# Kernel optimization log

Hardware: AMD Instinct MI355X
Metric: run time of the kernel (lower is better)

## Reference

```python
import math
import jax, jax.numpy as jnp
import numpy as np

B, S, D = 1, 1024, 2048
E, TOPK, H, DK, CONV = 8, 2, 6, 256, 4
DV = 2 * DK            # expand_v = 2
KD, VD = H * DK, H * DV
EPS = 1e-5
CAP_LEN = math.ceil(S * TOPK / TOPK * 1.0)  # capacity = 1.0 -> S


def setup_inputs() -> dict:
    key = jax.random.key(0)
    ks = jax.random.split(key, 16)
    sd = 0.02
    dt = jnp.exp(jax.random.uniform(ks[8], (H,)) * (math.log(0.1) - math.log(0.001)) + math.log(0.001))
    dt = jnp.clip(dt, 1e-4, None)
    dt_bias = dt + jnp.log(-jnp.expm1(-dt))
    return {
        'hidden_states': jax.random.normal(ks[0], (B, S, D), jnp.float32),
        'q_w': jax.random.normal(ks[1], (D, KD), jnp.float32) * sd,
        'gate_w': jax.random.normal(ks[2], (D, E), jnp.float32) * sd,
        'k_w': jax.random.normal(ks[3], (E, D, KD), jnp.float32) * sd,
        'v_w': jax.random.normal(ks[4], (E, D, VD), jnp.float32) * sd,
        'b_w': jax.random.normal(ks[5], (E, D, H), jnp.float32) * sd,
        'a_w': jax.random.normal(ks[6], (E, D, H), jnp.float32) * sd,
        'A_log': jnp.log(jax.random.uniform(ks[7], (H,), minval=1e-2, maxval=16.0)),
        'dt_bias': dt_bias,
        'q_conv_w': jax.random.normal(ks[9], (KD, CONV), jnp.float32) * 0.1,
        'k_conv_w': jax.random.normal(ks[10], (KD, CONV), jnp.float32) * 0.1,
        'v_conv_w': jax.random.normal(ks[11], (VD, CONV), jnp.float32) * 0.1,
        'g_w': jax.random.normal(ks[12], (D, VD), jnp.float32) * sd,
        'norm_w': jnp.ones((DV,), jnp.float32),
        'o_w': jax.random.normal(ks[13], (VD, D), jnp.float32) * sd,
    }


def _short_conv(x, w):
    # depthwise causal conv1d + silu. x: (N,T,C), w: (C,K)
    N, T, C = x.shape
    K = w.shape[1]
    y = jax.lax.conv_general_dilated(x.transpose(0, 2, 1), w[:, None, :], (1,),
                                     [(K - 1, 0)], feature_group_count=C)
    return jax.nn.silu(y.transpose(0, 2, 1))


def _l2norm(x):
    return x * jax.lax.rsqrt((x * x).sum(-1, keepdims=True) + 1e-6)


def reference(hidden_states, q_w, gate_w, k_w, v_w, b_w, a_w, A_log, dt_bias,
              q_conv_w, k_conv_w, v_conv_w, g_w, norm_w, o_w):
    b, s, d = B, S, D
    s_exp = s * TOPK
    # ---- router: softmax -> topk -> renormalize ----
    probs = jax.nn.softmax(hidden_states @ gate_w, axis=-1)        # (b,s,E)
    rw, sel = jax.lax.top_k(probs, TOPK)                           # (b,s,K)
    rw = rw / rw.sum(-1, keepdims=True)
    routing_mask = jax.nn.one_hot(sel, E, dtype=jnp.int32).sum(2)  # (b,s,E)
    # ---- transform(): dispatch tokens into per-expert capacity buffers ----
    x_rep = jnp.repeat(hidden_states, TOPK, axis=1)                # (b,s*K,d)
    sel_flat = sel.reshape(-1)
    batch_idx = jnp.repeat(jnp.arange(b), s_exp)
    sorted_indices = jnp.argsort(batch_idx * E + sel_flat)         # stable sort keeps temporal order
    x_sorted = x_rep.reshape(-1, d)[sorted_indices]
    counts = routing_mask.sum(1)                                   # (b,E) tokens per (batch,expert)
    flat_off = (jnp.cumsum(counts, 1) + (jnp.arange(b) * s_exp)[:, None]).reshape(-1)
    starts = jnp.concatenate([jnp.zeros((1,), flat_off.dtype), flat_off[:-1]])
    idx = jnp.arange(CAP_LEN)[None, :] + starts[:, None]
    trunc = idx + counts.reshape(-1)[:, None] - CAP_LEN            # right-align, drop overflow
    valid = (trunc < flat_off[:, None]) & (trunc >= 0) & (trunc >= starts[:, None])
    trunc = jnp.where(valid, trunc, 0)                             # (b*E, CAP_LEN)
    xe = x_sorted[trunc.reshape(-1)] * valid.reshape(-1)[:, None]
    xe = xe.reshape(b, E, CAP_LEN, d).transpose(1, 0, 2, 3)        # (E,b,T,d)
    T = CAP_LEN
    # ---- per-expert projections ----
    q = jnp.einsum('ebtd,dk->ebtk', xe, q_w)
    k = jnp.einsum('ebtd,edk->ebtk', xe, k_w)
    v = jnp.einsum('ebtd,edk->ebtk', xe, v_w)
    beta = jax.nn.sigmoid(jnp.einsum('ebtd,edh->ebth', xe, b_w))
    g = -jnp.exp(A_log) * jax.nn.softplus(jnp.einsum('ebtd,edh->ebth', xe, a_w) + dt_bias)
    # ---- short conv + silu, head split, qk l2 norm ----
    N = E * b
    q = _short_conv(q.reshape(N, T, KD), q_conv_w).reshape(N, T, H, DK)
    k = _short_conv(k.reshape(N, T, KD), k_conv_w).reshape(N, T, H, DK)
    v = _short_conv(v.reshape(N, T, VD), v_conv_w).reshape(N, T, H, DV)
    q = _l2norm(q) * (DK ** -0.5)
    k = _l2norm(k)
    beta = beta.reshape(N, T, H)
    g = g.reshape(N, T, H)
    # ---- gated delta rule recurrence: S_t = a_t S + beta_t k_t (v_t - a_t S^T k_t)^T ----
    def step(Sst, inp):
        q_t, k_t, v_t, b_t, g_t = inp
        Sst = Sst * jnp.exp(g_t)[..., None, None]
        pred = jnp.einsum('nhk,nhkv->nhv', k_t, Sst)
        delta = (v_t - pred) * b_t[..., None]
        Sst = Sst + jnp.einsum('nhk,nhv->nhkv', k_t, delta)
        o_t = jnp.einsum('nhk,nhkv->nhv', q_t, Sst)
        return Sst, o_t
    xs = (q.transpose(1, 0, 2, 3), k.transpose(1, 0, 2, 3), v.transpose(1, 0, 2, 3),
          beta.transpose(1, 0, 2), g.transpose(1, 0, 2))
    S0 = jnp.zeros((N, H, DK, DV), q.dtype)
    _, o = jax.lax.scan(step, S0, xs)                              # (T,N,H,DV)
    o = o.transpose(1, 0, 2, 3).reshape(E, b, T, H, DV)
    # ---- reconstruct(): scatter back and combine with routing weights ----
    re = o.transpose(1, 0, 2, 3, 4).reshape(b * E * T, H, DV)
    re = re * valid.reshape(-1)[:, None, None]
    resorted = jnp.zeros((b * s_exp, H, DV), re.dtype).at[trunc.reshape(-1)].add(re)
    restored = resorted[jnp.argsort(sorted_indices)].reshape(b, s, TOPK, H, DV)
    o_comb = (restored * rw[..., None, None]).sum(2)               # (b,s,H,DV)
    # ---- gated RMSNorm (swish gate) + output projection ----
    gg = (hidden_states @ g_w).reshape(b, s, H, DV)
    rms = o_comb * jax.lax.rsqrt((o_comb * o_comb).mean(-1, keepdims=True) + EPS)
    o_out = rms * norm_w * (gg * jax.nn.sigmoid(gg))
    return o_out.reshape(b, s, VD) @ o_w
```

## Files before the change

### kernel.cpp

```cpp
#include <hip/hip_runtime.h>
#include <math.h>

#define Dm    2048
#define Hh    6
#define DKk   256
#define DVv   512
#define KD    1536
#define VD    3072
#define QGW   4608
#define CH    4

typedef __attribute__((ext_vector_type(8))) __bf16 bf16x8;
typedef __attribute__((ext_vector_type(4))) float floatx4;

__device__ __forceinline__ unsigned short f2bf(float f) {
    unsigned int u = __float_as_uint(f);
    u = (u + 0x7fffu + ((u >> 16) & 1u)) >> 16;
    return (unsigned short)u;
}

__device__ __forceinline__ void gl_lds16(const void* g, void* l) {
    __builtin_amdgcn_global_load_lds((const __attribute__((address_space(1))) void*)g,
                                     (__attribute__((address_space(3))) void*)l, 16, 0, 0);
}

__global__ void router_kernel(const float* __restrict__ hidden,
                              const float* __restrict__ gate_w,
                              int* __restrict__ sel01, float* __restrict__ w01)
{
    int t = blockIdx.x;
    int lane = threadIdx.x;
    const float* hr = hidden + (size_t)t * Dm;
    float h[32];
#pragma unroll
    for (int i = 0; i < 32; ++i) h[i] = hr[lane + 64 * i];
    float logit[8];
#pragma unroll
    for (int e = 0; e < 8; ++e) {
        float acc = 0.f;
#pragma unroll
        for (int i = 0; i < 32; ++i) acc += h[i] * gate_w[(size_t)(lane + 64 * i) * 8 + e];
#pragma unroll
        for (int off = 1; off < 64; off <<= 1) acc += __shfl_xor(acc, off, 64);
        logit[e] = acc;
    }
    if (lane == 0) {
        int i0 = 0;
#pragma unroll
        for (int e = 1; e < 8; ++e) if (logit[e] > logit[i0]) i0 = e;
        int i1 = (i0 == 0) ? 1 : 0;
#pragma unroll
        for (int e = 0; e < 8; ++e) if (e != i0 && logit[e] > logit[i1]) i1 = e;
        float w0 = 1.f / (1.f + expf(logit[i1] - logit[i0]));
        sel01[2 * t] = i0; sel01[2 * t + 1] = i1;
        w01[2 * t] = w0;   w01[2 * t + 1] = 1.f - w0;
    }
}

__global__ void dispatch_kernel(const int* __restrict__ sel01,
                                int* __restrict__ list_c, int* __restrict__ posg,
                                int* __restrict__ cnt, int* __restrict__ basearr)
{
    __shared__ int wbase[16];
    __shared__ int sbase;
    int t = threadIdx.x;
    int lane = t & 63, w = t >> 6;
    int s0 = sel01[2 * t], s1 = sel01[2 * t + 1];
    if (t == 0) sbase = 0;
    __syncthreads();
    for (int e = 0; e < 8; ++e) {
        int flag  = (s0 == e || s1 == e) ? 1 : 0;
        int kslot = (s0 == e) ? 0 : 1;
        unsigned long long m = __ballot(flag);
        int lpre = __popcll(m & ((1ull << lane) - 1ull));
        if (lane == 0) wbase[w] = __popcll(m);
        __syncthreads();
        if (t == 0) {
            int run = sbase;
            basearr[e] = run;
            for (int i = 0; i < 16; ++i) { int tv = wbase[i]; wbase[i] = run; run += tv; }
            cnt[e] = run - sbase;
            sbase = run;
        }
        __syncthreads();
        if (flag) {
            int pos = wbase[w] + lpre;
            list_c[pos] = t;
            posg[2 * t + kslot] = pos;
        }
        __syncthreads();
    }
}

__global__ void cast_bf16_kernel(const float* __restrict__ x, unsigned short* __restrict__ y)
{
    int i = (blockIdx.x * 256 + threadIdx.x) * 4;
    float4 a = *(const float4*)(x + i);
    ushort4 o;
    o.x = f2bf(a.x); o.y = f2bf(a.y); o.z = f2bf(a.z); o.w = f2bf(a.w);
    *(ushort4*)(y + i) = o;
}

__global__ void gather_cast_kernel(const float* __restrict__ hidden, const int* __restrict__ list,
                                   unsigned short* __restrict__ xe)
{
    int slot = blockIdx.x;
    int tok = list[slot];
    const float* src = hidden + (size_t)tok * Dm;
    unsigned short* dst = xe + (size_t)slot * Dm;
    int c = threadIdx.x * 8;
    float4 a = *(const float4*)(src + c);
    float4 b = *(const float4*)(src + c + 4);
    ushort4 o1, o2;
    o1.x = f2bf(a.x); o1.y = f2bf(a.y); o1.z = f2bf(a.z); o1.w = f2bf(a.w);
    o2.x = f2bf(b.x); o2.y = f2bf(b.y); o2.z = f2bf(b.z); o2.w = f2bf(b.w);
    *(ushort4*)(dst + c) = o1;
    *(ushort4*)(dst + c + 4) = o2;
}

__global__ void transpose_cast_kernel(const float* __restrict__ in, unsigned short* __restrict__ out,
                                      int K, int N, size_t estride)
{
    __shared__ float tile[32][33];
    int b = blockIdx.z;
    int k0 = blockIdx.x * 32, n0 = blockIdx.y * 32;
    const float* ip = in + (size_t)b * K * N;
    unsigned short* op = out + (size_t)b * estride;
    int tx = threadIdx.x & 31, ty = threadIdx.x >> 5;
#pragma unroll
    for (int i = 0; i < 4; ++i)
        tile[ty + i * 8][tx] = ip[(size_t)(k0 + ty + i * 8) * N + n0 + tx];
    __syncthreads();
    int kq = threadIdx.x & 7, n = threadIdx.x >> 3;
    ushort4 o;
    o.x = f2bf(tile[kq * 4 + 0][n]);
    o.y = f2bf(tile[kq * 4 + 1][n]);
    o.z = f2bf(tile[kq * 4 + 2][n]);
    o.w = f2bf(tile[kq * 4 + 3][n]);
    *(ushort4*)(op + (size_t)(n0 + n) * K + k0 + kq * 4) = o;
}

template<bool EXPERT>
__global__ __launch_bounds__(256)
void gemm_bf16(const unsigned short* __restrict__ A,
               const unsigned short* __restrict__ Bt,
               float* __restrict__ C,
               const int* __restrict__ cnt, const int* __restrict__ basearr,
               int M, int K, int N)
{
    int e = EXPERT ? blockIdx.z : 0;
    int Mloc = M, base = 0;
    if (EXPERT) {
        Mloc = cnt[e]; base = basearr[e];
        if ((int)(blockIdx.x * 128) >= Mloc) return;
    }
    int m0 = blockIdx.x * 128, n0 = blockIdx.y * 128;
    const unsigned short* Ab = A + (size_t)base * K;
    const unsigned short* Bb = Bt + (size_t)e * (size_t)K * N;
    __shared__ unsigned short As[4][128 * 32];
    __shared__ unsigned short Bs[4][128 * 32];
    int tid = threadIdx.x;
    int lane = tid & 63, wave = tid >> 6;
    const unsigned short* ga[2];
    const unsigned short* gb[2];
    int lo[2];
#pragma unroll
    for (int j = 0; j < 2; ++j) {
        int flat = j * 256 + tid;
        int row = flat >> 2, sub = flat & 3;
        int ar = m0 + row; if (ar > Mloc - 1) ar = Mloc - 1;
        ga[j] = Ab + (size_t)ar * K + sub * 8;
        gb[j] = Bb + (size_t)(n0 + row) * K + sub * 8;
        lo[j] = flat * 8;
    }
    floatx4 acc[4][4];
#pragma unroll
    for (int i = 0; i < 4; ++i)
#pragma unroll
        for (int j = 0; j < 4; ++j) acc[i][j] = (floatx4){0.f, 0.f, 0.f, 0.f};

    int wm = (wave >> 1) * 64, wn = (wave & 1) * 64;
    int fr = lane & 15, kr = (lane >> 4) * 8;

    int nk = K >> 5;
    auto stage = [&](int buf, int t) {
        int k0 = t << 5;
        gl_lds16(ga[0] + k0, As[buf] + lo[0]);
        gl_lds16(gb[0] + k0, Bs[buf] + lo[0]);
        gl_lds16(ga[1] + k0, As[buf] + lo[1]);
        gl_lds16(gb[1] + k0, Bs[buf] + lo[1]);
    };
    stage(0, 0);
    stage(1, 1);
    stage(2, 2);
    int cur = 0;
    for (int t = 0; t < nk; ++t) {
        int nxt = (cur + 3) & 3;
        if (t + 3 < nk) stage(nxt, t + 3);
        int ahead = nk - 1 - t;
        if (ahead >= 3)      asm volatile("s_waitcnt vmcnt(12)\n\ts_barrier" ::: "memory");
        else if (ahead == 2) asm volatile("s_waitcnt vmcnt(8)\n\ts_barrier" ::: "memory");
        else if (ahead == 1) asm volatile("s_waitcnt vmcnt(4)\n\ts_barrier" ::: "memory");
        else                 asm volatile("s_waitcnt vmcnt(0)\n\ts_barrier" ::: "memory");
        bf16x8 af[4], bfr[4];
        const unsigned short* Ac = As[cur];
        const unsigned short* Bc = Bs[cur];
#pragma unroll
        for (int f = 0; f < 4; ++f) {
            af[f]  = *(const bf16x8*)(Ac + (size_t)(wm + f * 16 + fr) * 32 + kr);
            bfr[f] = *(const bf16x8*)(Bc + (size_t)(wn + f * 16 + fr) * 32 + kr);
        }
#pragma unroll
        for (int fm = 0; fm < 4; ++fm)
#pragma unroll
            for (int fn = 0; fn < 4; ++fn)
                acc[fm][fn] = __builtin_amdgcn_mfma_f32_16x16x32_bf16(af[fm], bfr[fn], acc[fm][fn], 0, 0, 0);
        asm volatile("s_waitcnt lgkmcnt(0)\n\ts_barrier" ::: "memory");
        cur = (cur + 1) & 3;
    }
    int rb = (lane >> 4) * 4;
#pragma unroll
    for (int fm = 0; fm < 4; ++fm) {
#pragma unroll
        for (int r = 0; r < 4; ++r) {
            int m = m0 + wm + fm * 16 + rb + r;
            if (m < Mloc) {
                float* cp = C + (size_t)(base + m) * N + n0 + wn + fr;
#pragma unroll
                for (int fn = 0; fn < 4; ++fn)
                    cp[fn * 16] = acc[fm][fn][r];
            }
        }
    }
}

__global__ void ba_kernel(const float* __restrict__ hidden,
                          const float* __restrict__ b_w, const float* __restrict__ a_w,
                          const float* __restrict__ A_log, const float* __restrict__ dt_bias,
                          const int* __restrict__ list, const int* __restrict__ cnt,
                          const int* __restrict__ basearr,
                          float* __restrict__ beta_c, float* __restrict__ g_c)
{
    int j = blockIdx.x, e = blockIdx.y;
    if (j >= cnt[e]) return;
    int gpos = basearr[e] + j;
    int tok = list[gpos];
    int lane = threadIdx.x;
    const float* hr = hidden + (size_t)tok * Dm;
    float h[32];
#pragma unroll
    for (int i = 0; i < 32; ++i) h[i] = hr[lane + 64 * i];
    for (int c = 0; c < 12; ++c) {
        int col = c % 6;
        const float* W = ((c < 6) ? b_w : a_w) + (size_t)e * Dm * 6;
        float acc = 0.f;
#pragma unroll
        for (int i = 0; i < 32; ++i) acc += h[i] * W[(size_t)(lane + 64 * i) * 6 + col];
#pragma unroll
        for (int off = 1; off < 64; off <<= 1) acc += __shfl_xor(acc, off, 64);
        if (lane == 0) {
            if (c < 6) {
                beta_c[gpos * 6 + col] = 1.f / (1.f + expf(-acc));
            } else {
                float x = acc + dt_bias[col];
                float sp = (x > 20.f) ? x : log1pf(expf(x));
                g_c[gpos * 6 + col] = -expf(A_log[col]) * sp;
            }
        }
    }
}

template<bool GATHER>
__global__ void conv_norm_kernel(const float* __restrict__ X, int xstride,
                                 const float* __restrict__ convw,
                                 const int* __restrict__ list, const int* __restrict__ cnt,
                                 const int* __restrict__ basearr,
                                 float* __restrict__ outb, float scale)
{
    int j = blockIdx.x, e = blockIdx.y, h = blockIdx.z;
    if (j >= cnt[e]) return;
    int base = basearr[e];
    int gpos = base + j;
    int c = h * DKk + threadIdx.x;
    float acc = 0.f;
#pragma unroll
    for (int tau = 0; tau < 4; ++tau) {
        int jj = j - 3 + tau;
        if (jj >= 0) {
            const float* row = GATHER ? (X + (size_t)list[base + jj] * xstride)
                                      : (X + (size_t)(base + jj) * xstride);
            acc += row[c] * convw[c * 4 + tau];
        }
    }
    float y = acc / (1.f + expf(-acc));
    float v = y * y;
#pragma unroll
    for (int off = 1; off < 64; off <<= 1) v += __shfl_xor(v, off, 64);
    __shared__ float red[4];
    if ((threadIdx.x & 63) == 0) red[threadIdx.x >> 6] = v;
    __syncthreads();
    float total = red[0] + red[1] + red[2] + red[3];
    outb[(size_t)gpos * KD + c] = y * rsqrtf(total + 1e-6f) * scale;
}

__global__ void conv_v_kernel(const float* __restrict__ X,
                              const float* __restrict__ convw,
                              const int* __restrict__ cnt, const int* __restrict__ basearr,
                              float* __restrict__ outb)
{
    int j = blockIdx.x, e = blockIdx.y;
    if (j >= cnt[e]) return;
    int base = basearr[e];
    int gpos = base + j;
    int c = blockIdx.z * 256 + threadIdx.x;
    float acc = 0.f;
#pragma unroll
    for (int tau = 0; tau < 4; ++tau) {
        int jj = j - 3 + tau;
        if (jj >= 0) acc += X[(size_t)(base + jj) * QGW + KD + c] * convw[c * 4 + tau];
    }
    outb[(size_t)gpos * VD + c] = acc / (1.f + expf(-acc));
}

__global__ void qk_kernel(const float* __restrict__ qn, const float* __restrict__ kn,
                          float* __restrict__ qk_c)
{
    int gpos = blockIdx.x, h = blockIdx.y;
    int lane = threadIdx.x;
    const float4* qp = (const float4*)(qn + (size_t)gpos * KD + h * DKk);
    const float4* kp = (const float4*)(kn + (size_t)gpos * KD + h * DKk);
    float4 a = qp[lane], b = kp[lane];
    float acc = a.x * b.x + a.y * b.y + a.z * b.z + a.w * b.w;
#pragma unroll
    for (int off = 1; off < 64; off <<= 1) acc += __shfl_xor(acc, off, 64);
    if (lane == 0) qk_c[(size_t)gpos * Hh + h] = acc;
}

__global__ __launch_bounds__(256, 3)
void recurrence_kernel(const float* __restrict__ qn, const float* __restrict__ kn,
                       const float* __restrict__ vc,
                       const float* __restrict__ beta_c, const float* __restrict__ g_c,
                       const float* __restrict__ qk_c,
                       const int* __restrict__ cnt, const int* __restrict__ basearr,
                       float* __restrict__ o_c)
{
    int vb = blockIdx.x, h = blockIdx.y, e = blockIdx.z;
    int n = cnt[e], base = basearr[e];
    if (n <= 0) return;
    int tid = threadIdx.x;
    int kpart = tid & 7, vcol = tid >> 3;
    int v = vb * 32 + vcol;
    int wv = tid >> 6, lane = tid & 63;

    __shared__ float lk[2][CH][256];
    __shared__ float lq[2][CH][256];

    const float* kb = kn + (size_t)base * KD + h * DKk;
    const float* qb = qn + (size_t)base * KD + h * DKk;
    const float* vp = vc + (size_t)base * VD + h * DVv + v;
    const float* gp = g_c    + (size_t)base * Hh + h;
    const float* bp = beta_c + (size_t)base * Hh + h;
    const float* xp = qk_c   + (size_t)base * Hh + h;
    float* op = o_c + (size_t)base * VD + h * DVv + v;

    float4 s[8];
#pragma unroll
    for (int i = 0; i < 8; ++i) s[i] = make_float4(0.f, 0.f, 0.f, 0.f);

    int nch = (n + CH - 1) / CH;

    auto stageKQ = [&](int buf, int c) {
        int jj = c * CH + wv; if (jj > n - 1) jj = n - 1;
        gl_lds16(kb + (size_t)jj * KD + lane * 4, &lk[buf][wv][lane * 4]);
        gl_lds16(qb + (size_t)jj * KD + lane * 4, &lq[buf][wv][lane * 4]);
    };

    float vA[CH], gA[CH], bA[CH], xA[CH];
    float vB[CH], gB[CH], bB[CH], xB[CH];

    auto loadScal = [&](float (&V)[CH], float (&G)[CH], float (&B)[CH], float (&X)[CH], int c) {
#pragma unroll
        for (int u = 0; u < CH; ++u) {
            int jj = c * CH + u; if (jj > n - 1) jj = n - 1;
            V[u] = vp[(size_t)jj * VD];
            G[u] = gp[(size_t)jj * Hh];
            B[u] = bp[(size_t)jj * Hh];
            X[u] = xp[(size_t)jj * Hh];
        }
    };

    auto computeChunk = [&](const float (&Lk)[CH][256], const float (&Lq)[CH][256],
                            const float (&V)[CH], const float (&G)[CH],
                            const float (&B)[CH], const float (&X)[CH], int c) {
#pragma unroll
        for (int u = 0; u < CH; ++u) {
            const float* Lku = &Lk[u][kpart * 4];
            const float* Lqu = &Lq[u][kpart * 4];
            float4 pa0 = make_float4(0.f,0.f,0.f,0.f), pa1 = make_float4(0.f,0.f,0.f,0.f);
            float4 ra0 = make_float4(0.f,0.f,0.f,0.f), ra1 = make_float4(0.f,0.f,0.f,0.f);
            float4 kk[8];
#pragma unroll
            for (int i = 0; i < 8; ++i) {
                kk[i] = *(const float4*)(Lku + i * 32);
                float4 qq = *(const float4*)(Lqu + i * 32);
                float4& pa = (i & 1) ? pa1 : pa0;
                float4& ra = (i & 1) ? ra1 : ra0;
                pa.x = fmaf(kk[i].x, s[i].x, pa.x); pa.y = fmaf(kk[i].y, s[i].y, pa.y);
                pa.z = fmaf(kk[i].z, s[i].z, pa.z); pa.w = fmaf(kk[i].w, s[i].w, pa.w);
                ra.x = fmaf(qq.x, s[i].x, ra.x); ra.y = fmaf(qq.y, s[i].y, ra.y);
                ra.z = fmaf(qq.z, s[i].z, ra.z); ra.w = fmaf(qq.w, s[i].w, ra.w);
            }
            float p = ((pa0.x + pa1.x) + (pa0.y + pa1.y)) + ((pa0.z + pa1.z) + (pa0.w + pa1.w));
            float r = ((ra0.x + ra1.x) + (ra0.y + ra1.y)) + ((ra0.z + ra1.z) + (ra0.w + ra1.w));
#pragma unroll
            for (int m = 1; m < 8; m <<= 1) {
                p += __shfl_xor(p, m, 64);
                r += __shfl_xor(r, m, 64);
            }
            float eg = __expf(G[u]);
            float delta = (V[u] - p * eg) * B[u];
            float out = fmaf(X[u], delta, eg * r);
#pragma unroll
            for (int i = 0; i < 8; ++i) {
                s[i].x = fmaf(eg, s[i].x, kk[i].x * delta);
                s[i].y = fmaf(eg, s[i].y, kk[i].y * delta);
                s[i].z = fmaf(eg, s[i].z, kk[i].z * delta);
                s[i].w = fmaf(eg, s[i].w, kk[i].w * delta);
            }
            int j = c * CH + u;
            if (kpart == 0 && j < n) op[(size_t)j * VD] = out;
        }
    };

    stageKQ(0, 0);
    loadScal(vA, gA, bA, xA, 0);
    stageKQ(1, 1);
    asm volatile("s_waitcnt vmcnt(2)\n\ts_barrier" ::: "memory");

    for (int c = 0; c < nch; c += 2) {
        loadScal(vB, gB, bB, xB, c + 1);
        computeChunk(lk[0], lq[0], vA, gA, bA, xA, c);
        __syncthreads();
        stageKQ(0, c + 2);
        asm volatile("s_waitcnt vmcnt(2)\n\ts_barrier" ::: "memory");
        if (c + 1 >= nch) break;
        loadScal(vA, gA, bA, xA, c + 2);
        computeChunk(lk[1], lq[1], vB, gB, bB, xB, c + 1);
        __syncthreads();
        stageKQ(1, c + 3);
        asm volatile("s_waitcnt vmcnt(2)\n\ts_barrier" ::: "memory");
    }
    asm volatile("s_waitcnt vmcnt(0)" ::: "memory");
}

__global__ void combine_kernel(const float* __restrict__ o_c, const float* __restrict__ qg,
                               const float* __restrict__ norm_w,
                               const int* __restrict__ posg, const float* __restrict__ w01,
                               unsigned short* __restrict__ ocg)
{
    int t = blockIdx.x, h = blockIdx.y;
    int p0 = posg[2 * t], p1 = posg[2 * t + 1];
    float w0 = w01[2 * t], w1 = w01[2 * t + 1];
    int v0 = threadIdx.x, v1 = threadIdx.x + 256;
    size_t r0 = (size_t)p0 * VD + h * DVv, r1 = (size_t)p1 * VD + h * DVv;
    float a  = w0 * o_c[r0 + v0] + w1 * o_c[r1 + v0];
    float b2 = w0 * o_c[r0 + v1] + w1 * o_c[r1 + v1];
    float val = a * a + b2 * b2;
#pragma unroll
    for (int off = 1; off < 64; off <<= 1) val += __shfl_xor(val, off, 64);
    __shared__ float red[4];
    if ((threadIdx.x & 63) == 0) red[threadIdx.x >> 6] = val;
    __syncthreads();
    float total = red[0] + red[1] + red[2] + red[3];
    float rms = rsqrtf(total / 512.f + 1e-5f);
    size_t og = (size_t)t * VD + h * DVv;
    size_t gq = (size_t)t * QGW + KD + h * DVv;
    float g0 = qg[gq + v0], g1 = qg[gq + v1];
    ocg[og + v0] = f2bf(a  * rms * norm_w[v0] * g0 / (1.f + expf(-g0)));
    ocg[og + v1] = f2bf(b2 * rms * norm_w[v1] * g1 / (1.f + expf(-g1)));
}

extern "C" void kernel_launch(void* const* d_in, const int* in_sizes, int n_in,
                              void* d_out, int out_size, void* d_ws, size_t ws_size,
                              hipStream_t stream)
{
    const float* hidden   = (const float*)d_in[0];
    const float* q_w      = (const float*)d_in[1];
    const float* gate_w   = (const float*)d_in[2];
    const float* k_w      = (const float*)d_in[3];
    const float* v_w      = (const float*)d_in[4];
    const float* b_w      = (const float*)d_in[5];
    const float* a_w      = (const float*)d_in[6];
    const float* A_log    = (const float*)d_in[7];
    const float* dt_bias  = (const float*)d_in[8];
    const float* q_conv_w = (const float*)d_in[9];
    const float* k_conv_w = (const float*)d_in[10];
    const float* v_conv_w = (const float*)d_in[11];
    const float* g_w      = (const float*)d_in[12];
    const float* norm_w   = (const float*)d_in[13];
    const float* o_w      = (const float*)d_in[14];
    float* outp = (float*)d_out;

    float* f = (float*)d_ws;
    size_t off = 0;
    auto alloc = [&](size_t n) { float* p = f + off; off += (n + 3) & ~(size_t)3; return p; };
    float* qg     = alloc((size_t)1024 * QGW);
    float* kvraw  = alloc((size_t)2048 * QGW);
    float* qn     = alloc((size_t)2048 * 1536);
    float* kn     = alloc((size_t)2048 * 1536);
    float* vconv  = alloc((size_t)2048 * 3072);
    float* o_c    = alloc((size_t)2048 * 3072);
    float* beta_c = alloc(2048 * 6);
    float* g_c    = alloc(2048 * 6);
    float* qk_c   = alloc(2048 * 6);
    float* w01f   = alloc(2048);

    unsigned short* u = (unsigned short*)(f + off);
    size_t uoff = 0;
    auto ualloc = [&](size_t n) { unsigned short* p = u + uoff; uoff += (n + 7) & ~(size_t)7; return p; };
    unsigned short* hidden_bf = ualloc((size_t)1024 * 2048);
    unsigned short* xe_c      = ualloc((size_t)2048 * 2048);
    unsigned short* ocg       = ualloc((size_t)1024 * 3072);
    unsigned short* qg_wT     = ualloc((size_t)QGW * 2048);
    unsigned short* kv_wT     = ualloc((size_t)8 * QGW * 2048);
    unsigned short* o_wT      = ualloc((size_t)3072 * 2048);

    int* ib      = (int*)(u + uoff);
    int* sel01   = ib;
    int* list_c  = ib + 2048;
    int* posg    = ib + 4096;
    int* cnt     = ib + 6144;
    int* basearr = ib + 6152;

    const size_t EST = (size_t)2048 * QGW;

    router_kernel<<<1024, 64, 0, stream>>>(hidden, gate_w, sel01, w01f);
    dispatch_kernel<<<1, 1024, 0, stream>>>(sel01, list_c, posg, cnt, basearr);

    cast_bf16_kernel<<<2048, 256, 0, stream>>>(hidden, hidden_bf);
    gather_cast_kernel<<<2048, 256, 0, stream>>>(hidden, list_c, xe_c);
    transpose_cast_kernel<<<dim3(64, 48, 1), 256, 0, stream>>>(q_w, qg_wT, 2048, 1536, 0);
    transpose_cast_kernel<<<dim3(64, 96, 1), 256, 0, stream>>>(g_w, qg_wT + (size_t)1536 * 2048, 2048, 3072, 0);
    transpose_cast_kernel<<<dim3(64, 48, 8), 256, 0, stream>>>(k_w, kv_wT, 2048, 1536, EST);
    transpose_cast_kernel<<<dim3(64, 96, 8), 256, 0, stream>>>(v_w, kv_wT + (size_t)1536 * 2048, 2048, 3072, EST);
    transpose_cast_kernel<<<dim3(96, 64, 1), 256, 0, stream>>>(o_w, o_wT, 3072, 2048, 0);

    gemm_bf16<false><<<dim3(8, 36), 256, 0, stream>>>(hidden_bf, qg_wT, qg, nullptr, nullptr, 1024, 2048, QGW);
    gemm_bf16<true ><<<dim3(8, 36, 8), 256, 0, stream>>>(xe_c, kv_wT, kvraw, cnt, basearr, 0, 2048, QGW);

    ba_kernel<<<dim3(1024, 8), 64, 0, stream>>>(hidden, b_w, a_w, A_log, dt_bias,
                                                list_c, cnt, basearr, beta_c, g_c);

    conv_norm_kernel<true ><<<dim3(1024, 8, 6), 256, 0, stream>>>(qg,    QGW, q_conv_w, list_c, cnt, basearr, qn, 0.0625f);
    conv_norm_kernel<false><<<dim3(1024, 8, 6), 256, 0, stream>>>(kvraw, QGW, k_conv_w, list_c, cnt, basearr, kn, 1.0f);
    conv_v_kernel<<<dim3(1024, 8, 12), 256, 0, stream>>>(kvraw, v_conv_w, cnt, basearr, vconv);

    qk_kernel<<<dim3(2048, 6), 64, 0, stream>>>(qn, kn, qk_c);

    recurrence_kernel<<<dim3(16, 6, 8), 256, 0, stream>>>(qn, kn, vconv, beta_c, g_c, qk_c,
                                                          cnt, basearr, o_c);

    combine_kernel<<<dim3(1024, 6), 256, 0, stream>>>(o_c, qg, norm_w, posg, w01f, ocg);
    gemm_bf16<false><<<dim3(8, 16), 256, 0, stream>>>(ocg, o_wT, outp, nullptr, nullptr, 1024, 3072, 2048);
}
```

Baseline: 1.233 ms.

## Swizzle GEMM LDS tiles and use double buffering for expert GEMM

Applies an XOR swizzle to the 16-byte k-chunks stored in LDS, permuting the global source addresses and the fragment read offsets to match, so MFMA fragment reads hit fewer LDS bank conflicts. The expert-variant GEMM also drops from four to two LDS buffers, which halves its shared memory so more blocks can be resident per CU. The cost is a shallower prefetch pipeline for the expert GEMMs, with waits placed closer to the loads.

```diff
diff --git a/kernel.cpp b/kernel.cpp
--- a/kernel.cpp
+++ b/kernel.cpp
@@ -148,6 +148,7 @@
                const int* __restrict__ cnt, const int* __restrict__ basearr,
                int M, int K, int N)
 {
+    constexpr int NBUF = EXPERT ? 2 : 4;
     int e = EXPERT ? blockIdx.z : 0;
     int Mloc = M, base = 0;
     if (EXPERT) {
@@ -157,8 +158,8 @@
     int m0 = blockIdx.x * 128, n0 = blockIdx.y * 128;
     const unsigned short* Ab = A + (size_t)base * K;
     const unsigned short* Bb = Bt + (size_t)e * (size_t)K * N;
-    __shared__ unsigned short As[4][128 * 32];
-    __shared__ unsigned short Bs[4][128 * 32];
+    __shared__ unsigned short As[NBUF][128 * 32];
+    __shared__ unsigned short Bs[NBUF][128 * 32];
     int tid = threadIdx.x;
     int lane = tid & 63, wave = tid >> 6;
     const unsigned short* ga[2];
@@ -168,9 +169,10 @@
     for (int j = 0; j < 2; ++j) {
         int flat = j * 256 + tid;
         int row = flat >> 2, sub = flat & 3;
+        int subs = sub ^ ((row >> 1) & 3);
         int ar = m0 + row; if (ar > Mloc - 1) ar = Mloc - 1;
-        ga[j] = Ab + (size_t)ar * K + sub * 8;
-        gb[j] = Bb + (size_t)(n0 + row) * K + sub * 8;
+        ga[j] = Ab + (size_t)ar * K + subs * 8;
+        gb[j] = Bb + (size_t)(n0 + row) * K + subs * 8;
         lo[j] = flat * 8;
     }
     floatx4 acc[4][4];
@@ -180,8 +182,8 @@
         for (int j = 0; j < 4; ++j) acc[i][j] = (floatx4){0.f, 0.f, 0.f, 0.f};
 
     int wm = (wave >> 1) * 64, wn = (wave & 1) * 64;
-    int fr = lane & 15, kr = (lane >> 4) * 8;
-
+    int fr = lane & 15, q = lane >> 4;
+    int qs = q ^ ((fr >> 1) & 3);
     int nk = K >> 5;
     auto stage = [&](int buf, int t) {
         int k0 = t << 5;
@@ -190,25 +192,29 @@
         gl_lds16(ga[1] + k0, As[buf] + lo[1]);
         gl_lds16(gb[1] + k0, Bs[buf] + lo[1]);
     };
-    stage(0, 0);
-    stage(1, 1);
-    stage(2, 2);
+#pragma unroll
+    for (int b = 0; b < NBUF - 1; ++b) stage(b, b);
     int cur = 0;
     for (int t = 0; t < nk; ++t) {
-        int nxt = (cur + 3) & 3;
-        if (t + 3 < nk) stage(nxt, t + 3);
+        int nxt = cur + (NBUF - 1); if (nxt >= NBUF) nxt -= NBUF;
+        if (t + NBUF - 1 < nk) stage(nxt, t + NBUF - 1);
         int ahead = nk - 1 - t;
-        if (ahead >= 3)      asm volatile("s_waitcnt vmcnt(12)\n\ts_barrier" ::: "memory");
-        else if (ahead == 2) asm volatile("s_waitcnt vmcnt(8)\n\ts_barrier" ::: "memory");
-        else if (ahead == 1) asm volatile("s_waitcnt vmcnt(4)\n\ts_barrier" ::: "memory");
-        else                 asm volatile("s_waitcnt vmcnt(0)\n\ts_barrier" ::: "memory");
+        if constexpr (EXPERT) {
+            if (ahead >= 1)      asm volatile("s_waitcnt vmcnt(4)\n\ts_barrier" ::: "memory");
+            else                 asm volatile("s_waitcnt vmcnt(0)\n\ts_barrier" ::: "memory");
+        } else {
+            if (ahead >= 3)      asm volatile("s_waitcnt vmcnt(12)\n\ts_barrier" ::: "memory");
+            else if (ahead == 2) asm volatile("s_waitcnt vmcnt(8)\n\ts_barrier" ::: "memory");
+            else if (ahead == 1) asm volatile("s_waitcnt vmcnt(4)\n\ts_barrier" ::: "memory");
+            else                 asm volatile("s_waitcnt vmcnt(0)\n\ts_barrier" ::: "memory");
+        }
         bf16x8 af[4], bfr[4];
         const unsigned short* Ac = As[cur];
         const unsigned short* Bc = Bs[cur];
 #pragma unroll
         for (int f = 0; f < 4; ++f) {
-            af[f]  = *(const bf16x8*)(Ac + (size_t)(wm + f * 16 + fr) * 32 + kr);
-            bfr[f] = *(const bf16x8*)(Bc + (size_t)(wn + f * 16 + fr) * 32 + kr);
+            af[f]  = *(const bf16x8*)(Ac + (size_t)(wm + f * 16 + fr) * 32 + qs * 8);
+            bfr[f] = *(const bf16x8*)(Bc + (size_t)(wn + f * 16 + fr) * 32 + qs * 8);
         }
 #pragma unroll
         for (int fm = 0; fm < 4; ++fm)
@@ -216,9 +222,9 @@
             for (int fn = 0; fn < 4; ++fn)
                 acc[fm][fn] = __builtin_amdgcn_mfma_f32_16x16x32_bf16(af[fm], bfr[fn], acc[fm][fn], 0, 0, 0);
         asm volatile("s_waitcnt lgkmcnt(0)\n\ts_barrier" ::: "memory");
-        cur = (cur + 1) & 3;
-    }
-    int rb = (lane >> 4) * 4;
+        cur = cur + 1 == NBUF ? 0 : cur + 1;
+    }
+    int rb = q * 4;
 #pragma unroll
     for (int fm = 0; fm < 4; ++fm) {
 #pragma unroll
```

Result: faster. 1.184 ms (-4.0%).
